# Optimization experiments

Hardware: AMD Instinct MI355X
Metric: run time of the kernel (lower is better)

Reference implementation:

```python
import jax, jax.numpy as jnp
import numpy as np

N = 50000   # nodes
E = 409600  # edges
H = 2       # heads
C = 64      # per-head channels


def _seg_softmax(alpha, dst, n):
    # PyG-style softmax over edges grouped by destination node. alpha: [E, H]
    m = jax.ops.segment_max(alpha, dst, num_segments=n)
    m = jnp.where(jnp.isfinite(m), m, 0.0)
    ex = jnp.exp(alpha - m[dst])
    s = jax.ops.segment_sum(ex, dst, num_segments=n)
    return ex / (s[dst] + 1e-16)


def _tconv(x, src, dst, e, Wq, bq, Wk, bk, Wv, bv, We, Ws, bs, n):
    # PyG TransformerConv (concat=True, beta=False, root_weight=True, dropout=0)
    q = (x @ Wq + bq).reshape(n, H, C)
    k = (x @ Wk + bk).reshape(n, H, C)
    v = (x @ Wv + bv).reshape(n, H, C)
    eh = (e @ We).reshape(-1, H, C)          # lin_edge has no bias in PyG
    kj = k[src] + eh                          # [E, H, C]
    alpha = (q[dst] * kj).sum(-1) / jnp.sqrt(jnp.float32(C))  # [E, H]
    alpha = _seg_softmax(alpha, dst, n)
    msg = (v[src] + eh) * alpha[:, :, None]   # [E, H, C]
    out = jax.ops.segment_sum(msg, dst, num_segments=n).reshape(n, H * C)
    return out + x @ Ws + bs                  # root/skip connection


def setup_inputs() -> dict:
    key = jax.random.key(0)
    ks = jax.random.split(key, 32)

    def lin_w(k, i, o):
        return (jax.random.normal(k, (i, o), dtype=jnp.float32) / np.sqrt(i)).astype(jnp.float32)

    inp = {
        "x": jax.random.normal(ks[0], (N, 6), dtype=jnp.float32),
        "edge_index": jax.random.randint(ks[1], (2, E), 0, N, dtype=jnp.int32).astype(jnp.int64),
        "edge_attr": jax.random.normal(ks[2], (E, 1), dtype=jnp.float32),
        # edge encoder: Linear(1, 64)
        "We_enc": lin_w(ks[3], 1, 64), "be_enc": jnp.zeros((64,), jnp.float32),
        # conv1: TransformerConv(6, 64, heads=2, edge_dim=64)
        "Wq1": lin_w(ks[4], 6, H * C), "bq1": jnp.zeros((H * C,), jnp.float32),
        "Wk1": lin_w(ks[5], 6, H * C), "bk1": jnp.zeros((H * C,), jnp.float32),
        "Wv1": lin_w(ks[6], 6, H * C), "bv1": jnp.zeros((H * C,), jnp.float32),
        "We1": lin_w(ks[7], 64, H * C),
        "Ws1": lin_w(ks[8], 6, H * C), "bs1": jnp.zeros((H * C,), jnp.float32),
        # conv2: TransformerConv(128, 64, heads=2, edge_dim=64)
        "Wq2": lin_w(ks[9], 128, H * C), "bq2": jnp.zeros((H * C,), jnp.float32),
        "Wk2": lin_w(ks[10], 128, H * C), "bk2": jnp.zeros((H * C,), jnp.float32),
        "Wv2": lin_w(ks[11], 128, H * C), "bv2": jnp.zeros((H * C,), jnp.float32),
        "We2": lin_w(ks[12], 64, H * C),
        "Ws2": lin_w(ks[13], 128, H * C), "bs2": jnp.zeros((H * C,), jnp.float32),
        # fc: Linear(128, 1)
        "Wfc": lin_w(ks[14], 128, 1), "bfc": jnp.zeros((1,), jnp.float32),
    }
    return inp


def reference(x, edge_index, edge_attr,
              We_enc, be_enc,
              Wq1, bq1, Wk1, bk1, Wv1, bv1, We1, Ws1, bs1,
              Wq2, bq2, Wk2, bk2, Wv2, bv2, We2, Ws2, bs2,
              Wfc, bfc):
    src, dst = edge_index[0], edge_index[1]
    e = edge_attr @ We_enc + be_enc           # [E, 64]
    h = jax.nn.relu(_tconv(x, src, dst, e, Wq1, bq1, Wk1, bk1, Wv1, bv1, We1, Ws1, bs1, N))
    h = jax.nn.relu(_tconv(h, src, dst, e, Wq2, bq2, Wk2, bk2, Wv2, bv2, We2, Ws2, bs2, N))
    return h @ Wfc + bfc                      # [N, 1]
```

## Files before the change

### kernel.cpp

```cpp
#include <hip/hip_runtime.h>


#define HC 128

typedef __attribute__((ext_vector_type(8))) short bf16x8;
typedef __attribute__((ext_vector_type(4))) float f32x4;
#if __has_builtin(__builtin_amdgcn_fdot2_f32_bf16)
typedef __attribute__((ext_vector_type(2))) __bf16 bf16x2;
#define HAS_DOT2 1
#else
#define HAS_DOT2 0
#endif

__device__ __forceinline__ unsigned bf16_rne(float f) {
    unsigned u = __float_as_uint(f);
    return (u + 0x7fffu + ((u >> 16) & 1u)) >> 16;
}
__device__ __forceinline__ float blo(unsigned u) { return __uint_as_float(u << 16); }
__device__ __forceinline__ float bhi(unsigned u) { return __uint_as_float(u & 0xffff0000u); }

__global__ void k_uc(const float* __restrict__ We_enc, const float* __restrict__ be_enc,
                     const float* __restrict__ We1, const float* __restrict__ We2,
                     float* __restrict__ uc) {
    int c = threadIdx.x;
    float u1 = 0.f, c1 = 0.f, u2 = 0.f, c2 = 0.f;
    for (int j = 0; j < 64; ++j) {
        float we = We_enc[j], be = be_enc[j];
        float w1 = We1[j * HC + c], w2 = We2[j * HC + c];
        u1 += we * w1; c1 += be * w1;
        u2 += we * w2; c2 += be * w2;
    }
    uc[c] = u1; uc[HC + c] = c1; uc[2 * HC + c] = u2; uc[3 * HC + c] = c2;
}

__global__ __launch_bounds__(256) void k_wpack(
    const float* __restrict__ Wq, const float* __restrict__ Wk,
    const float* __restrict__ Wv, const float* __restrict__ Ws,
    unsigned short* __restrict__ Bph) {
    int t = blockIdx.x * 256 + threadIdx.x;
    int nn = t >> 7;
    int kk = t & 127;
    int mat = nn >> 7, c = nn & 127;
    const float* W = (mat == 0) ? Wq : (mat == 1) ? Wk : (mat == 2) ? Wv : Ws;
    Bph[nn * 128 + kk] = (unsigned short)bf16_rne(W[kk * 128 + c]);
}

__global__ __launch_bounds__(256) void k_hist(const int* __restrict__ ei, int* __restrict__ deg, int E) {
    int t = blockIdx.x * blockDim.x + threadIdx.x;
    if (t < E) atomicAdd(&deg[ei[E + t]], 1);
}

__global__ __launch_bounds__(256) void k_scan1(const int* __restrict__ deg, int* __restrict__ bsum, int n) {
    int t = blockIdx.x * 256 + threadIdx.x;
    int v = (t < n) ? deg[t] : 0;
#pragma unroll
    for (int off = 1; off < 64; off <<= 1) v += __shfl_xor(v, off);
    __shared__ int wsum[4];
    int lane = threadIdx.x & 63, w = threadIdx.x >> 6;
    if (lane == 0) wsum[w] = v;
    __syncthreads();
    if (threadIdx.x == 0) bsum[blockIdx.x] = wsum[0] + wsum[1] + wsum[2] + wsum[3];
}

__global__ __launch_bounds__(256) void k_scan2(int* __restrict__ bsum, int nb) {
    __shared__ int sh[256];
    int t = threadIdx.x;
    int v = (t < nb) ? bsum[t] : 0;
    sh[t] = v;
    __syncthreads();
    for (int off = 1; off < 256; off <<= 1) {
        int x = (t >= off) ? sh[t - off] : 0;
        __syncthreads();
        sh[t] += x;
        __syncthreads();
    }
    if (t < nb) bsum[t] = sh[t] - v;
}

__global__ __launch_bounds__(256) void k_scan3(int* __restrict__ deg, const int* __restrict__ bsum,
                                               int* __restrict__ rowptr, int n, int E) {
    int t = blockIdx.x * 256 + threadIdx.x;
    int tid = threadIdx.x;
    int v = (t < n) ? deg[t] : 0;
    __shared__ int sh[256];
    sh[tid] = v;
    __syncthreads();
    for (int off = 1; off < 256; off <<= 1) {
        int x = (tid >= off) ? sh[tid - off] : 0;
        __syncthreads();
        sh[tid] += x;
        __syncthreads();
    }
    if (t < n) { rowptr[t] = bsum[blockIdx.x] + sh[tid] - v; deg[t] = 0; }
    if (t == 0) rowptr[n] = E;
}

__global__ __launch_bounds__(256) void k_scatter(const int* __restrict__ ei, const int* __restrict__ rowptr,
                                                 int* __restrict__ cursor, int* __restrict__ eid, int E) {
    int t = blockIdx.x * blockDim.x + threadIdx.x;
    if (t >= E) return;
    int dst = ei[E + t];
    int pos = rowptr[dst] + atomicAdd(&cursor[dst], 1);
    eid[pos] = t;
}

__global__ __launch_bounds__(256) void k_bsortg(
    const int* __restrict__ rowptr, int* __restrict__ eid,
    const int* __restrict__ ei, const float* __restrict__ ea,
    int* __restrict__ srcs, float* __restrict__ eas, int n) {
    int t = blockIdx.x * blockDim.x + threadIdx.x;
    if (t >= n) return;
    int b = rowptr[t], e = rowptr[t + 1];
    for (int i = b + 1; i < e; ++i) {
        int key = eid[i];
        int j = i - 1;
        while (j >= b && eid[j] > key) { eid[j + 1] = eid[j]; --j; }
        eid[j + 1] = key;
    }
    for (int i = b; i < e; ++i) {
        int id = eid[i];
        srcs[i] = ei[id];
        eas[i] = ea[id];
    }
}

__global__ __launch_bounds__(256) void k_lin6(
    const float* __restrict__ X, int n,
    const float* __restrict__ Wq, const float* __restrict__ bq,
    const float* __restrict__ Wk, const float* __restrict__ bk,
    const float* __restrict__ Wv, const float* __restrict__ bv,
    const float* __restrict__ Ws, const float* __restrict__ bs,
    unsigned short* __restrict__ q16, unsigned short* __restrict__ kv,
    float* __restrict__ o) {
    __shared__ float xs[16][6];
    const int base = blockIdx.x * 16;
    const int tid = threadIdx.x;
    for (int i = tid; i < 16 * 6; i += 256) {
        int ni = base + i / 6;
        xs[i / 6][i % 6] = (ni < n) ? X[(size_t)ni * 6 + (i % 6)] : 0.f;
    }
    __syncthreads();
    const int c = tid & 127;
    const int m = tid >> 7;
    const float* WA = m ? Wv : Wq;
    const float* WB = m ? Ws : Wk;
    float accA[16], accB[16];
#pragma unroll
    for (int i = 0; i < 16; ++i) { accA[i] = 0.f; accB[i] = 0.f; }
    for (int j = 0; j < 6; ++j) {
        float w0 = WA[j * HC + c];
        float w1 = WB[j * HC + c];
#pragma unroll
        for (int i = 0; i < 16; ++i) {
            float xv = xs[i][j];
            accA[i] += xv * w0;
            accB[i] += xv * w1;
        }
    }
    if (m == 0) {
        const float bA = bq[c], bB = bk[c];
#pragma unroll
        for (int i = 0; i < 16; ++i) {
            int ni = base + i;
            if (ni < n) {
                q16[(size_t)ni * HC + c] = (unsigned short)bf16_rne(accA[i] + bA);
                kv[(size_t)ni * 256 + c] = (unsigned short)bf16_rne(accB[i] + bB);
            }
        }
    } else {
        const float bA = bv[c], bB = bs[c];
#pragma unroll
        for (int i = 0; i < 16; ++i) {
            int ni = base + i;
            if (ni < n) {
                kv[(size_t)ni * 256 + 128 + c] = (unsigned short)bf16_rne(accA[i] + bA);
                o[(size_t)ni * HC + c] = accB[i] + bB;
            }
        }
    }
}

__global__ __launch_bounds__(256, 4) void k_lin2(
    const unsigned short* __restrict__ hb, const unsigned short* __restrict__ Bph,
    const float* __restrict__ bq, const float* __restrict__ bk,
    const float* __restrict__ bv, const float* __restrict__ bs,
    unsigned short* __restrict__ q16, unsigned short* __restrict__ kv,
    float* __restrict__ o, int n) {
    __shared__ unsigned short Bs[128][128];
    const int tid = threadIdx.x;
    const int wid = tid >> 6, l = tid & 63;
    const int la = l & 15, lk = l >> 4;
    const int mb = blockIdx.x * 64;
    int nodeA = mb + wid * 16 + la;
    if (nodeA >= n) nodeA = n - 1;
    const int sw = (la & 7) << 3;
    const int crow0 = mb + wid * 16 + lk * 4;

    bf16x8 areg[4];
#pragma unroll
    for (int ks = 0; ks < 4; ++ks)
        areg[ks] = *(const bf16x8*)&hb[(size_t)nodeA * 128 + lk * 8 + ks * 32];

    for (int cq = 0; cq < 4; ++cq) {
        if (cq) __syncthreads();
        for (int i = tid; i < 128 * 16; i += 256) {
            int kk8 = i & 15;
            int nnl = i >> 4;
            bf16x8 val = *(const bf16x8*)&Bph[((size_t)(cq * 128 + nnl)) * 128 + kk8 * 8];
            int swk = (kk8 ^ (nnl & 7)) * 8;
            *(bf16x8*)&Bs[nnl][swk] = val;
        }
        __syncthreads();

        f32x4 acc[8];
#pragma unroll
        for (int nt = 0; nt < 8; ++nt) acc[nt] = (f32x4){0.f, 0.f, 0.f, 0.f};
#pragma unroll
        for (int ks = 0; ks < 4; ++ks) {
            const int rk = (lk * 8 + ks * 32) ^ sw;
#pragma unroll
            for (int nt = 0; nt < 8; ++nt) {
                bf16x8 Bh = *(const bf16x8*)&Bs[nt * 16 + la][rk];
                acc[nt] = __builtin_amdgcn_mfma_f32_16x16x32_bf16(areg[ks], Bh, acc[nt], 0, 0, 0);
            }
        }
        const float* bias = (cq == 0) ? bq : (cq == 1) ? bk : (cq == 2) ? bv : bs;
#pragma unroll
        for (int nt = 0; nt < 8; ++nt) {
            const int col = nt * 16 + la;
            const float bb = bias[col];
            if (cq == 3) {
#pragma unroll
                for (int j = 0; j < 4; ++j) {
                    int n0 = crow0 + j;
                    if (n0 < n) o[(size_t)n0 * 128 + col] = acc[nt][j] + bb;
                }
            } else if (cq == 0) {
#pragma unroll
                for (int j = 0; j < 4; ++j) {
                    int n0 = crow0 + j;
                    if (n0 < n) q16[(size_t)n0 * 128 + col] = (unsigned short)bf16_rne(acc[nt][j] + bb);
                }
            } else {
                const int co = (cq == 1) ? col : 128 + col;
#pragma unroll
                for (int j = 0; j < 4; ++j) {
                    int n0 = crow0 + j;
                    if (n0 < n) kv[(size_t)n0 * 256 + co] = (unsigned short)bf16_rne(acc[nt][j] + bb);
                }
            }
        }
    }
}

template <int MODE>
__global__ __launch_bounds__(256) void k_attn(
    const unsigned short* __restrict__ q16, const unsigned short* __restrict__ kvp,
    const int* __restrict__ rowptr, const int* __restrict__ srcs, const float* __restrict__ eas,
    const float* __restrict__ ucu, const float* __restrict__ ucc,
    const float* __restrict__ io, unsigned short* __restrict__ hb,
    const float* __restrict__ Wfc, const float* __restrict__ bfc,
    float* __restrict__ out, int n) {
    int wid = (int)((blockIdx.x * (size_t)blockDim.x + threadIdx.x) >> 6);
    int lane = threadIdx.x & 63;
    if (wid >= n) return;
    const int half = lane >> 5;
    const int sub = (lane >> 4) & 1;
    const int grp = lane >> 4;
    const int hl = lane & 15;
    const int ch = hl * 8;
    const int strm = half + 2 * sub;

    uint4 qp = *(const uint4*)&q16[(size_t)wid * 128 + ch];
    float qf0 = blo(qp.x), qf1 = bhi(qp.x), qf2 = blo(qp.y), qf3 = bhi(qp.y);
    float qf4 = blo(qp.z), qf5 = bhi(qp.z), qf6 = blo(qp.w), qf7 = bhi(qp.w);
    float4 uuA = *(const float4*)&ucu[ch], uuB = *(const float4*)&ucu[ch + 4];
    float4 ccA = *(const float4*)&ucc[ch], ccB = *(const float4*)&ucc[ch + 4];

    float qu = qf0 * uuA.x + qf1 * uuA.y + qf2 * uuA.z + qf3 * uuA.w
             + qf4 * uuB.x + qf5 * uuB.y + qf6 * uuB.z + qf7 * uuB.w;
    float qc = qf0 * ccA.x + qf1 * ccA.y + qf2 * ccA.z + qf3 * ccA.w
             + qf4 * ccB.x + qf5 * ccB.y + qf6 * ccB.z + qf7 * ccB.w;
#pragma unroll
    for (int off = 1; off < 8; off <<= 1) {
        qu += __shfl_xor(qu, off);
        qc += __shfl_xor(qc, off);
    }

    int b = rowptr[wid], e = rowptr[wid + 1];
    float m = -3.0e38f, s = 0.f, sea = 0.f;
    float av0 = 0.f, av1 = 0.f, av2 = 0.f, av3 = 0.f;
    float av4 = 0.f, av5 = 0.f, av6 = 0.f, av7 = 0.f;

    if (b < e) {
        int pi = b + strm;
        bool val = pi < e;
        int pc = val ? pi : e - 1;
        int src = srcs[pc];
        float eav = eas[pc];
        const unsigned short* row = &kvp[(size_t)src * 256 + ch];
        uint4 ku = *(const uint4*)row;
        uint4 vu = *(const uint4*)(row + 128);
        for (int p = b; p < e; p += 4) {
            int pn = p + 4 + strm;
            bool valn = pn < e;
            int pcn = valn ? pn : e - 1;
            int srcn = srcs[pcn];
            float eavn = eas[pcn];
            const unsigned short* rown = &kvp[(size_t)srcn * 256 + ch];
            uint4 kun = *(const uint4*)rown;
            uint4 vun = *(const uint4*)(rown + 128);

            float d;
#if HAS_DOT2
            d = __builtin_amdgcn_fdot2_f32_bf16(
                    __builtin_bit_cast(bf16x2, ku.x), __builtin_bit_cast(bf16x2, qp.x),
                __builtin_amdgcn_fdot2_f32_bf16(
                    __builtin_bit_cast(bf16x2, ku.y), __builtin_bit_cast(bf16x2, qp.y),
                __builtin_amdgcn_fdot2_f32_bf16(
                    __builtin_bit_cast(bf16x2, ku.z), __builtin_bit_cast(bf16x2, qp.z),
                __builtin_amdgcn_fdot2_f32_bf16(
                    __builtin_bit_cast(bf16x2, ku.w), __builtin_bit_cast(bf16x2, qp.w),
                    0.f, false), false), false), false);
#else
            d = qf0 * blo(ku.x) + qf1 * bhi(ku.x) + qf2 * blo(ku.y) + qf3 * bhi(ku.y)
              + qf4 * blo(ku.z) + qf5 * bhi(ku.z) + qf6 * blo(ku.w) + qf7 * bhi(ku.w);
#endif
            d += __shfl_xor(d, 1); d += __shfl_xor(d, 2); d += __shfl_xor(d, 4);
            float a = val ? (d + fmaf(eav, qu, qc)) * 0.125f : -INFINITY;
            float nm = fmaxf(m, a);
            float sc = __expf(m - nm);
            float pw = __expf(a - nm);
            s = fmaf(s, sc, pw);
            sea = fmaf(sea, sc, pw * eav);
            av0 = fmaf(av0, sc, pw * blo(vu.x));
            av1 = fmaf(av1, sc, pw * bhi(vu.x));
            av2 = fmaf(av2, sc, pw * blo(vu.y));
            av3 = fmaf(av3, sc, pw * bhi(vu.y));
            av4 = fmaf(av4, sc, pw * blo(vu.z));
            av5 = fmaf(av5, sc, pw * bhi(vu.z));
            av6 = fmaf(av6, sc, pw * blo(vu.w));
            av7 = fmaf(av7, sc, pw * bhi(vu.w));
            m = nm;
            ku = kun; vu = vun; eav = eavn; val = valn;
        }
    }

#pragma unroll
    for (int M = 16; M <= 32; M <<= 1) {
        float om = __shfl_xor(m, M);
        float os = __shfl_xor(s, M);
        float osea = __shfl_xor(sea, M);
        float o0 = __shfl_xor(av0, M), o1 = __shfl_xor(av1, M);
        float o2 = __shfl_xor(av2, M), o3 = __shfl_xor(av3, M);
        float o4 = __shfl_xor(av4, M), o5 = __shfl_xor(av5, M);
        float o6 = __shfl_xor(av6, M), o7 = __shfl_xor(av7, M);
        float nm = fmaxf(m, om);
        float scS = __expf(m - nm);
        float scO = __expf(om - nm);
        s = s * scS + os * scO;
        sea = sea * scS + osea * scO;
        av0 = av0 * scS + o0 * scO; av1 = av1 * scS + o1 * scO;
        av2 = av2 * scS + o2 * scO; av3 = av3 * scS + o3 * scO;
        av4 = av4 * scS + o4 * scO; av5 = av5 * scS + o5 * scO;
        av6 = av6 * scS + o6 * scO; av7 = av7 * scS + o7 * scO;
        m = nm;
    }

    float inv = 1.f / (s + 1e-16f);
    float4 skA = *(const float4*)&io[(size_t)wid * 128 + ch];
    float4 skB = *(const float4*)&io[(size_t)wid * 128 + ch + 4];
    float r0 = fmaxf((av0 + uuA.x * sea + ccA.x * s) * inv + skA.x, 0.f);
    float r1 = fmaxf((av1 + uuA.y * sea + ccA.y * s) * inv + skA.y, 0.f);
    float r2 = fmaxf((av2 + uuA.z * sea + ccA.z * s) * inv + skA.z, 0.f);
    float r3 = fmaxf((av3 + uuA.w * sea + ccA.w * s) * inv + skA.w, 0.f);
    float r4 = fmaxf((av4 + uuB.x * sea + ccB.x * s) * inv + skB.x, 0.f);
    float r5 = fmaxf((av5 + uuB.y * sea + ccB.y * s) * inv + skB.y, 0.f);
    float r6 = fmaxf((av6 + uuB.z * sea + ccB.z * s) * inv + skB.z, 0.f);
    float r7 = fmaxf((av7 + uuB.w * sea + ccB.w * s) * inv + skB.w, 0.f);

    if (MODE == 1) {
        if (grp == 0) {
            uint4 hv;
            hv.x = bf16_rne(r0) | (bf16_rne(r1) << 16);
            hv.y = bf16_rne(r2) | (bf16_rne(r3) << 16);
            hv.z = bf16_rne(r4) | (bf16_rne(r5) << 16);
            hv.w = bf16_rne(r6) | (bf16_rne(r7) << 16);
            *(uint4*)&hb[(size_t)wid * 128 + ch] = hv;
        }
    } else {
        float4 wfA = *(const float4*)&Wfc[ch];
        float4 wfB = *(const float4*)&Wfc[ch + 4];
        float rr = r0 * wfA.x + r1 * wfA.y + r2 * wfA.z + r3 * wfA.w
                 + r4 * wfB.x + r5 * wfB.y + r6 * wfB.z + r7 * wfB.w;
#pragma unroll
        for (int off = 1; off < 16; off <<= 1) rr += __shfl_xor(rr, off);
        if (lane == 0) out[wid] = rr + bfc[0];
    }
}

extern "C" void kernel_launch(void* const* d_in, const int* in_sizes, int n_in,
                              void* d_out, int out_size, void* d_ws, size_t ws_size,
                              hipStream_t stream) {
    const float* x      = (const float*)d_in[0];
    const int*   ei     = (const int*)d_in[1];
    const float* ea     = (const float*)d_in[2];
    const float* We_enc = (const float*)d_in[3];
    const float* be_enc = (const float*)d_in[4];
    const float* Wq1 = (const float*)d_in[5],  *bq1 = (const float*)d_in[6];
    const float* Wk1 = (const float*)d_in[7],  *bk1 = (const float*)d_in[8];
    const float* Wv1 = (const float*)d_in[9],  *bv1 = (const float*)d_in[10];
    const float* We1 = (const float*)d_in[11];
    const float* Ws1 = (const float*)d_in[12], *bs1 = (const float*)d_in[13];
    const float* Wq2 = (const float*)d_in[14], *bq2 = (const float*)d_in[15];
    const float* Wk2 = (const float*)d_in[16], *bk2 = (const float*)d_in[17];
    const float* Wv2 = (const float*)d_in[18], *bv2 = (const float*)d_in[19];
    const float* We2 = (const float*)d_in[20];
    const float* Ws2 = (const float*)d_in[21], *bs2 = (const float*)d_in[22];
    const float* Wfc = (const float*)d_in[23], *bfc = (const float*)d_in[24];

    const int n = in_sizes[0] / 6;
    const int E = in_sizes[2];

    float* ws = (float*)d_ws;
    size_t off = 0;
    unsigned short* qb16 = (unsigned short*)(ws + off); off += (size_t)n * HC / 2;
    float* Bb = ws + off; off += (size_t)n * HC;
    unsigned short* kv16 = (unsigned short*)(ws + off); off += (size_t)n * HC;
    int* rowptr = (int*)(ws + off); off += (size_t)(n + 1);
    int* deg    = (int*)(ws + off); off += (size_t)n;
    int* bsum   = (int*)(ws + off); off += 256;
    int* eid    = (int*)(ws + off); off += (size_t)E;
    int* srcs   = (int*)(ws + off); off += (size_t)E;
    float* eas  = ws + off; off += (size_t)E;
    float* uc   = ws + off; off += 512;
    unsigned short* hb16 = (unsigned short*)(ws + off); off += (size_t)n * HC / 2;
    unsigned short* Bph = (unsigned short*)(ws + off); off += 512 * 128 / 2;

    const int eb = (E + 255) / 256;
    const int nb = (n + 255) / 256;
    const int wb = (int)(((size_t)n * 64 + 255) / 256);

    hipLaunchKernelGGL(k_uc, dim3(1), dim3(128), 0, stream, We_enc, be_enc, We1, We2, uc);
    hipLaunchKernelGGL(k_wpack, dim3(256), dim3(256), 0, stream, Wq2, Wk2, Wv2, Ws2, Bph);

    hipMemsetAsync(deg, 0, (size_t)n * sizeof(int), stream);
    hipLaunchKernelGGL(k_hist, dim3(eb), dim3(256), 0, stream, ei, deg, E);
    hipLaunchKernelGGL(k_scan1, dim3(nb), dim3(256), 0, stream, deg, bsum, n);
    hipLaunchKernelGGL(k_scan2, dim3(1), dim3(256), 0, stream, bsum, nb);
    hipLaunchKernelGGL(k_scan3, dim3(nb), dim3(256), 0, stream, deg, bsum, rowptr, n, E);
    hipLaunchKernelGGL(k_scatter, dim3(eb), dim3(256), 0, stream, ei, rowptr, deg, eid, E);
    hipLaunchKernelGGL(k_bsortg, dim3(nb), dim3(256), 0, stream, rowptr, eid, ei, ea, srcs, eas, n);

    hipLaunchKernelGGL(k_lin6, dim3((n + 15) / 16), dim3(256), 0, stream,
                       x, n, Wq1, bq1, Wk1, bk1, Wv1, bv1, Ws1, bs1, qb16, kv16, Bb);
    hipLaunchKernelGGL((k_attn<1>), dim3(wb), dim3(256), 0, stream,
                       qb16, kv16, rowptr, srcs, eas, uc, uc + HC, Bb, hb16,
                       Wfc, bfc, (float*)d_out, n);

    hipLaunchKernelGGL(k_lin2, dim3((n + 63) / 64), dim3(256), 0, stream,
                       hb16, Bph, bq2, bk2, bv2, bs2, qb16, kv16, Bb, n);
    hipLaunchKernelGGL((k_attn<0>), dim3(wb), dim3(256), 0, stream,
                       qb16, kv16, rowptr, srcs, eas, uc + 2 * HC, uc + 3 * HC, Bb,
                       (unsigned short*)nullptr, Wfc, bfc, (float*)d_out, n);
}
```

Before: 218.5 us.

## Drop per-node edge sort, store skip in bf16, deepen attention gather prefetch

The scatter kernel now writes source index and edge attribute straight into CSR order, which removes the per-node insertion sort and the eid buffer. Edge order within each destination then depends on atomic order, so floating-point summation order becomes nondeterministic. The root/skip term is stored as bf16 instead of fp32, which halves that traffic at some cost in precision. The attention loop prefetches two edge batches ahead instead of one, giving more memory-level parallelism for the K/V gathers at the cost of more registers.

```diff
diff --git a/kernel.cpp b/kernel.cpp
--- a/kernel.cpp
+++ b/kernel.cpp
@@ -95,33 +95,16 @@
     if (t == 0) rowptr[n] = E;
 }
 
-__global__ __launch_bounds__(256) void k_scatter(const int* __restrict__ ei, const int* __restrict__ rowptr,
-                                                 int* __restrict__ cursor, int* __restrict__ eid, int E) {
+__global__ __launch_bounds__(256) void k_scatter(
+    const int* __restrict__ ei, const float* __restrict__ ea,
+    const int* __restrict__ rowptr, int* __restrict__ cursor,
+    int* __restrict__ srcs, float* __restrict__ eas, int E) {
     int t = blockIdx.x * blockDim.x + threadIdx.x;
     if (t >= E) return;
     int dst = ei[E + t];
     int pos = rowptr[dst] + atomicAdd(&cursor[dst], 1);
-    eid[pos] = t;
-}
-
-__global__ __launch_bounds__(256) void k_bsortg(
-    const int* __restrict__ rowptr, int* __restrict__ eid,
-    const int* __restrict__ ei, const float* __restrict__ ea,
-    int* __restrict__ srcs, float* __restrict__ eas, int n) {
-    int t = blockIdx.x * blockDim.x + threadIdx.x;
-    if (t >= n) return;
-    int b = rowptr[t], e = rowptr[t + 1];
-    for (int i = b + 1; i < e; ++i) {
-        int key = eid[i];
-        int j = i - 1;
-        while (j >= b && eid[j] > key) { eid[j + 1] = eid[j]; --j; }
-        eid[j + 1] = key;
-    }
-    for (int i = b; i < e; ++i) {
-        int id = eid[i];
-        srcs[i] = ei[id];
-        eas[i] = ea[id];
-    }
+    srcs[pos] = ei[t];
+    eas[pos] = ea[t];
 }
 
 __global__ __launch_bounds__(256) void k_lin6(
@@ -131,7 +114,7 @@
     const float* __restrict__ Wv, const float* __restrict__ bv,
     const float* __restrict__ Ws, const float* __restrict__ bs,
     unsigned short* __restrict__ q16, unsigned short* __restrict__ kv,
-    float* __restrict__ o) {
+    unsigned short* __restrict__ sk) {
     __shared__ float xs[16][6];
     const int base = blockIdx.x * 16;
     const int tid = threadIdx.x;
@@ -174,7 +157,7 @@
             int ni = base + i;
             if (ni < n) {
                 kv[(size_t)ni * 256 + 128 + c] = (unsigned short)bf16_rne(accA[i] + bA);
-                o[(size_t)ni * HC + c] = accB[i] + bB;
+                sk[(size_t)ni * HC + c] = (unsigned short)bf16_rne(accB[i] + bB);
             }
         }
     }
@@ -185,7 +168,7 @@
     const float* __restrict__ bq, const float* __restrict__ bk,
     const float* __restrict__ bv, const float* __restrict__ bs,
     unsigned short* __restrict__ q16, unsigned short* __restrict__ kv,
-    float* __restrict__ o, int n) {
+    unsigned short* __restrict__ sk, int n) {
     __shared__ unsigned short Bs[128][128];
     const int tid = threadIdx.x;
     const int wid = tid >> 6, l = tid & 63;
@@ -229,17 +212,12 @@
         for (int nt = 0; nt < 8; ++nt) {
             const int col = nt * 16 + la;
             const float bb = bias[col];
-            if (cq == 3) {
+            if (cq == 0 || cq == 3) {
+                unsigned short* out = (cq == 0) ? q16 : sk;
 #pragma unroll
                 for (int j = 0; j < 4; ++j) {
                     int n0 = crow0 + j;
-                    if (n0 < n) o[(size_t)n0 * 128 + col] = acc[nt][j] + bb;
-                }
-            } else if (cq == 0) {
-#pragma unroll
-                for (int j = 0; j < 4; ++j) {
-                    int n0 = crow0 + j;
-                    if (n0 < n) q16[(size_t)n0 * 128 + col] = (unsigned short)bf16_rne(acc[nt][j] + bb);
+                    if (n0 < n) out[(size_t)n0 * 128 + col] = (unsigned short)bf16_rne(acc[nt][j] + bb);
                 }
             } else {
                 const int co = (cq == 1) ? col : 128 + col;
@@ -258,33 +236,32 @@
     const unsigned short* __restrict__ q16, const unsigned short* __restrict__ kvp,
     const int* __restrict__ rowptr, const int* __restrict__ srcs, const float* __restrict__ eas,
     const float* __restrict__ ucu, const float* __restrict__ ucc,
-    const float* __restrict__ io, unsigned short* __restrict__ hb,
+    const unsigned short* __restrict__ io, unsigned short* __restrict__ hb,
     const float* __restrict__ Wfc, const float* __restrict__ bfc,
     float* __restrict__ out, int n) {
     int wid = (int)((blockIdx.x * (size_t)blockDim.x + threadIdx.x) >> 6);
     int lane = threadIdx.x & 63;
     if (wid >= n) return;
-    const int half = lane >> 5;
-    const int sub = (lane >> 4) & 1;
     const int grp = lane >> 4;
     const int hl = lane & 15;
     const int ch = hl * 8;
-    const int strm = half + 2 * sub;
 
     uint4 qp = *(const uint4*)&q16[(size_t)wid * 128 + ch];
-    float qf0 = blo(qp.x), qf1 = bhi(qp.x), qf2 = blo(qp.y), qf3 = bhi(qp.y);
-    float qf4 = blo(qp.z), qf5 = bhi(qp.z), qf6 = blo(qp.w), qf7 = bhi(qp.w);
-    float4 uuA = *(const float4*)&ucu[ch], uuB = *(const float4*)&ucu[ch + 4];
-    float4 ccA = *(const float4*)&ucc[ch], ccB = *(const float4*)&ucc[ch + 4];
-
-    float qu = qf0 * uuA.x + qf1 * uuA.y + qf2 * uuA.z + qf3 * uuA.w
-             + qf4 * uuB.x + qf5 * uuB.y + qf6 * uuB.z + qf7 * uuB.w;
-    float qc = qf0 * ccA.x + qf1 * ccA.y + qf2 * ccA.z + qf3 * ccA.w
-             + qf4 * ccB.x + qf5 * ccB.y + qf6 * ccB.z + qf7 * ccB.w;
-#pragma unroll
-    for (int off = 1; off < 8; off <<= 1) {
-        qu += __shfl_xor(qu, off);
-        qc += __shfl_xor(qc, off);
+    float qu, qc;
+    {
+        float qf0 = blo(qp.x), qf1 = bhi(qp.x), qf2 = blo(qp.y), qf3 = bhi(qp.y);
+        float qf4 = blo(qp.z), qf5 = bhi(qp.z), qf6 = blo(qp.w), qf7 = bhi(qp.w);
+        float4 uA = *(const float4*)&ucu[ch], uB = *(const float4*)&ucu[ch + 4];
+        float4 cA = *(const float4*)&ucc[ch], cB = *(const float4*)&ucc[ch + 4];
+        qu = qf0 * uA.x + qf1 * uA.y + qf2 * uA.z + qf3 * uA.w
+           + qf4 * uB.x + qf5 * uB.y + qf6 * uB.z + qf7 * uB.w;
+        qc = qf0 * cA.x + qf1 * cA.y + qf2 * cA.z + qf3 * cA.w
+           + qf4 * cB.x + qf5 * cB.y + qf6 * cB.z + qf7 * cB.w;
+#pragma unroll
+        for (int off = 1; off < 8; off <<= 1) {
+            qu += __shfl_xor(qu, off);
+            qc += __shfl_xor(qc, off);
+        }
     }
 
     int b = rowptr[wid], e = rowptr[wid + 1];
@@ -293,56 +270,57 @@
     float av4 = 0.f, av5 = 0.f, av6 = 0.f, av7 = 0.f;
 
     if (b < e) {
-        int pi = b + strm;
-        bool val = pi < e;
-        int pc = val ? pi : e - 1;
-        int src = srcs[pc];
-        float eav = eas[pc];
-        const unsigned short* row = &kvp[(size_t)src * 256 + ch];
-        uint4 ku = *(const uint4*)row;
-        uint4 vu = *(const uint4*)(row + 128);
+        int p0 = b + grp;          bool v0 = p0 < e; int c0 = v0 ? p0 : e - 1;
+        int p1 = b + 4 + grp;      bool v1 = p1 < e; int c1 = v1 ? p1 : e - 1;
+        int s0 = srcs[c0], s1 = srcs[c1];
+        float ea0 = eas[c0], ea1 = eas[c1];
+        const unsigned short* r0p = &kvp[(size_t)s0 * 256 + ch];
+        const unsigned short* r1p = &kvp[(size_t)s1 * 256 + ch];
+        uint4 ku0 = *(const uint4*)r0p, vu0 = *(const uint4*)(r0p + 128);
+        uint4 ku1 = *(const uint4*)r1p, vu1 = *(const uint4*)(r1p + 128);
         for (int p = b; p < e; p += 4) {
-            int pn = p + 4 + strm;
-            bool valn = pn < e;
-            int pcn = valn ? pn : e - 1;
-            int srcn = srcs[pcn];
-            float eavn = eas[pcn];
-            const unsigned short* rown = &kvp[(size_t)srcn * 256 + ch];
-            uint4 kun = *(const uint4*)rown;
-            uint4 vun = *(const uint4*)(rown + 128);
+            int p2 = p + 8 + grp;
+            bool v2 = p2 < e; int c2 = v2 ? p2 : e - 1;
+            int s2 = srcs[c2];
+            float ea2 = eas[c2];
+            const unsigned short* r2p = &kvp[(size_t)s2 * 256 + ch];
+            uint4 ku2 = *(const uint4*)r2p, vu2 = *(const uint4*)(r2p + 128);
 
             float d;
 #if HAS_DOT2
             d = __builtin_amdgcn_fdot2_f32_bf16(
-                    __builtin_bit_cast(bf16x2, ku.x), __builtin_bit_cast(bf16x2, qp.x),
+                    __builtin_bit_cast(bf16x2, ku0.x), __builtin_bit_cast(bf16x2, qp.x),
                 __builtin_amdgcn_fdot2_f32_bf16(
-                    __builtin_bit_cast(bf16x2, ku.y), __builtin_bit_cast(bf16x2, qp.y),
+                    __builtin_bit_cast(bf16x2, ku0.y), __builtin_bit_cast(bf16x2, qp.y),
                 __builtin_amdgcn_fdot2_f32_bf16(
-                    __builtin_bit_cast(bf16x2, ku.z), __builtin_bit_cast(bf16x2, qp.z),
+                    __builtin_bit_cast(bf16x2, ku0.z), __builtin_bit_cast(bf16x2, qp.z),
                 __builtin_amdgcn_fdot2_f32_bf16(
-                    __builtin_bit_cast(bf16x2, ku.w), __builtin_bit_cast(bf16x2, qp.w),
+                    __builtin_bit_cast(bf16x2, ku0.w), __builtin_bit_cast(bf16x2, qp.w),
                     0.f, false), false), false), false);
 #else
-            d = qf0 * blo(ku.x) + qf1 * bhi(ku.x) + qf2 * blo(ku.y) + qf3 * bhi(ku.y)
-              + qf4 * blo(ku.z) + qf5 * bhi(ku.z) + qf6 * blo(ku.w) + qf7 * bhi(ku.w);
+            d = blo(qp.x) * blo(ku0.x) + bhi(qp.x) * bhi(ku0.x)
+              + blo(qp.y) * blo(ku0.y) + bhi(qp.y) * bhi(ku0.y)
+              + blo(qp.z) * blo(ku0.z) + bhi(qp.z) * bhi(ku0.z)
+              + blo(qp.w) * blo(ku0.w) + bhi(qp.w) * bhi(ku0.w);
 #endif
             d += __shfl_xor(d, 1); d += __shfl_xor(d, 2); d += __shfl_xor(d, 4);
-            float a = val ? (d + fmaf(eav, qu, qc)) * 0.125f : -INFINITY;
+            float a = v0 ? (d + fmaf(ea0, qu, qc)) * 0.125f : -INFINITY;
             float nm = fmaxf(m, a);
             float sc = __expf(m - nm);
             float pw = __expf(a - nm);
             s = fmaf(s, sc, pw);
-            sea = fmaf(sea, sc, pw * eav);
-            av0 = fmaf(av0, sc, pw * blo(vu.x));
-            av1 = fmaf(av1, sc, pw * bhi(vu.x));
-            av2 = fmaf(av2, sc, pw * blo(vu.y));
-            av3 = fmaf(av3, sc, pw * bhi(vu.y));
-            av4 = fmaf(av4, sc, pw * blo(vu.z));
-            av5 = fmaf(av5, sc, pw * bhi(vu.z));
-            av6 = fmaf(av6, sc, pw * blo(vu.w));
-            av7 = fmaf(av7, sc, pw * bhi(vu.w));
+            sea = fmaf(sea, sc, pw * ea0);
+            av0 = fmaf(av0, sc, pw * blo(vu0.x));
+            av1 = fmaf(av1, sc, pw * bhi(vu0.x));
+            av2 = fmaf(av2, sc, pw * blo(vu0.y));
+            av3 = fmaf(av3, sc, pw * bhi(vu0.y));
+            av4 = fmaf(av4, sc, pw * blo(vu0.z));
+            av5 = fmaf(av5, sc, pw * bhi(vu0.z));
+            av6 = fmaf(av6, sc, pw * blo(vu0.w));
+            av7 = fmaf(av7, sc, pw * bhi(vu0.w));
             m = nm;
-            ku = kun; vu = vun; eav = eavn; val = valn;
+            ku0 = ku1; vu0 = vu1; ea0 = ea1; v0 = v1;
+            ku1 = ku2; vu1 = vu2; ea1 = ea2; v1 = v2;
         }
     }
 
@@ -367,17 +345,18 @@
         m = nm;
     }
 
+    float4 uuA = *(const float4*)&ucu[ch], uuB = *(const float4*)&ucu[ch + 4];
+    float4 ccA = *(const float4*)&ucc[ch], ccB = *(const float4*)&ucc[ch + 4];
     float inv = 1.f / (s + 1e-16f);
-    float4 skA = *(const float4*)&io[(size_t)wid * 128 + ch];
-    float4 skB = *(const float4*)&io[(size_t)wid * 128 + ch + 4];
-    float r0 = fmaxf((av0 + uuA.x * sea + ccA.x * s) * inv + skA.x, 0.f);
-    float r1 = fmaxf((av1 + uuA.y * sea + ccA.y * s) * inv + skA.y, 0.f);
-    float r2 = fmaxf((av2 + uuA.z * sea + ccA.z * s) * inv + skA.z, 0.f);
-    float r3 = fmaxf((av3 + uuA.w * sea + ccA.w * s) * inv + skA.w, 0.f);
-    float r4 = fmaxf((av4 + uuB.x * sea + ccB.x * s) * inv + skB.x, 0.f);
-    float r5 = fmaxf((av5 + uuB.y * sea + ccB.y * s) * inv + skB.y, 0.f);
-    float r6 = fmaxf((av6 + uuB.z * sea + ccB.z * s) * inv + skB.z, 0.f);
-    float r7 = fmaxf((av7 + uuB.w * sea + ccB.w * s) * inv + skB.w, 0.f);
+    uint4 skp = *(const uint4*)&io[(size_t)wid * 128 + ch];
+    float r0 = fmaxf((av0 + uuA.x * sea + ccA.x * s) * inv + blo(skp.x), 0.f);
+    float r1 = fmaxf((av1 + uuA.y * sea + ccA.y * s) * inv + bhi(skp.x), 0.f);
+    float r2 = fmaxf((av2 + uuA.z * sea + ccA.z * s) * inv + blo(skp.y), 0.f);
+    float r3 = fmaxf((av3 + uuA.w * sea + ccA.w * s) * inv + bhi(skp.y), 0.f);
+    float r4 = fmaxf((av4 + uuB.x * sea + ccB.x * s) * inv + blo(skp.z), 0.f);
+    float r5 = fmaxf((av5 + uuB.y * sea + ccB.y * s) * inv + bhi(skp.z), 0.f);
+    float r6 = fmaxf((av6 + uuB.z * sea + ccB.z * s) * inv + blo(skp.w), 0.f);
+    float r7 = fmaxf((av7 + uuB.w * sea + ccB.w * s) * inv + bhi(skp.w), 0.f);
 
     if (MODE == 1) {
         if (grp == 0) {
@@ -425,12 +404,11 @@
     float* ws = (float*)d_ws;
     size_t off = 0;
     unsigned short* qb16 = (unsigned short*)(ws + off); off += (size_t)n * HC / 2;
-    float* Bb = ws + off; off += (size_t)n * HC;
+    unsigned short* sk16 = (unsigned short*)(ws + off); off += (size_t)n * HC / 2;
     unsigned short* kv16 = (unsigned short*)(ws + off); off += (size_t)n * HC;
     int* rowptr = (int*)(ws + off); off += (size_t)(n + 1);
     int* deg    = (int*)(ws + off); off += (size_t)n;
     int* bsum   = (int*)(ws + off); off += 256;
-    int* eid    = (int*)(ws + off); off += (size_t)E;
     int* srcs   = (int*)(ws + off); off += (size_t)E;
     float* eas  = ws + off; off += (size_t)E;
     float* uc   = ws + off; off += 512;
@@ -449,18 +427,17 @@
     hipLaunchKernelGGL(k_scan1, dim3(nb), dim3(256), 0, stream, deg, bsum, n);
     hipLaunchKernelGGL(k_scan2, dim3(1), dim3(256), 0, stream, bsum, nb);
     hipLaunchKernelGGL(k_scan3, dim3(nb), dim3(256), 0, stream, deg, bsum, rowptr, n, E);
-    hipLaunchKernelGGL(k_scatter, dim3(eb), dim3(256), 0, stream, ei, rowptr, deg, eid, E);
-    hipLaunchKernelGGL(k_bsortg, dim3(nb), dim3(256), 0, stream, rowptr, eid, ei, ea, srcs, eas, n);
+    hipLaunchKernelGGL(k_scatter, dim3(eb), dim3(256), 0, stream, ei, ea, rowptr, deg, srcs, eas, E);
 
     hipLaunchKernelGGL(k_lin6, dim3((n + 15) / 16), dim3(256), 0, stream,
-                       x, n, Wq1, bq1, Wk1, bk1, Wv1, bv1, Ws1, bs1, qb16, kv16, Bb);
+                       x, n, Wq1, bq1, Wk1, bk1, Wv1, bv1, Ws1, bs1, qb16, kv16, sk16);
     hipLaunchKernelGGL((k_attn<1>), dim3(wb), dim3(256), 0, stream,
-                       qb16, kv16, rowptr, srcs, eas, uc, uc + HC, Bb, hb16,
+                       qb16, kv16, rowptr, srcs, eas, uc, uc + HC, sk16, hb16,
                        Wfc, bfc, (float*)d_out, n);
 
     hipLaunchKernelGGL(k_lin2, dim3((n + 63) / 64), dim3(256), 0, stream,
-                       hb16, Bph, bq2, bk2, bv2, bs2, qb16, kv16, Bb, n);
+                       hb16, Bph, bq2, bk2, bv2, bs2, qb16, kv16, sk16, n);
     hipLaunchKernelGGL((k_attn<0>), dim3(wb), dim3(256), 0, stream,
-                       qb16, kv16, rowptr, srcs, eas, uc + 2 * HC, uc + 3 * HC, Bb,
+                       qb16, kv16, rowptr, srcs, eas, uc + 2 * HC, uc + 3 * HC, sk16,
                        (unsigned short*)nullptr, Wfc, bfc, (float*)d_out, n);
 }
```

Measured after the change: 199.1 us. -8.9%, faster.
